# Optimization experiments

Hardware: AMD Instinct MI355X
Metric: run time of the kernel (lower is better)

## Reference

```python
import jax, jax.numpy as jnp
import numpy as np


def _fake_quant(x, num_bits):
    # Per-tensor uniform min/max fake quantization with STE (straight-through).
    qmax = float(2 ** num_bits - 1)
    mn = jnp.min(x)
    mx = jnp.max(x)
    scale = (mx - mn) / qmax
    q = jnp.round((x - mn) / scale) * scale + mn
    return x + jax.lax.stop_gradient(q - x)


def _qlinear(x, W, b, num_bits):
    xq = _fake_quant(x, num_bits)
    Wq = _fake_quant(W, num_bits)
    return xq @ Wq.T + b


def setup_inputs() -> dict:
    key = jax.random.key(0)
    ks = jax.random.split(key, 7)
    B, D, H = 8192, 1024, 1024
    s = 1.0 / np.sqrt(H)
    return {
        "input": jax.random.normal(ks[0], (B, D), jnp.float32),
        "h": jax.random.normal(ks[1], (B, H), jnp.float32),
        "c": jax.random.normal(ks[2], (B, H), jnp.float32),
        "W_in": jax.random.normal(ks[3], (4 * H, D), jnp.float32) * s,
        "b_in": jax.random.normal(ks[4], (4 * H,), jnp.float32) * s,
        "W_h": jax.random.normal(ks[5], (4 * H, H), jnp.float32) * s,
        "b_h": jax.random.normal(ks[6], (4 * H,), jnp.float32) * s,
        "num_bits": 8,
        "num_bits_grad": 8,
    }


def reference(input, h, c, W_in, b_in, W_h, b_h, num_bits, num_bits_grad):
    B = input.shape[0]
    Hd = h.shape[1]
    mixed_input = _qlinear(input, W_in, b_in, num_bits).reshape(B, 4, Hd)
    mixed_hidden = _qlinear(h, W_h, b_h, num_bits).reshape(B, 4, Hd)
    gates = mixed_input + mixed_hidden  # [B, 4, H]
    i = jax.nn.sigmoid(gates[:, 0, :])
    f = jax.nn.sigmoid(gates[:, 1, :])
    g = jnp.tanh(gates[:, 2, :])
    o = jax.nn.sigmoid(gates[:, 3, :])
    c_ = f * c + i * g
    h_ = o * jnp.tanh(c_)
    return (h_, c_)
```

## Files before the change

### kernel.cpp

```cpp
#include <hip/hip_runtime.h>
#include <hip/hip_bf16.h>

typedef unsigned short u16;
typedef int i32x4 __attribute__((ext_vector_type(4)));
typedef signed char s8;

#define NB_RED 256

__global__ void k_minmax_partial(const float* __restrict__ x, const float* __restrict__ h,
                                 const float* __restrict__ wi, const float* __restrict__ wh,
                                 float* __restrict__ partials) {
    int t = blockIdx.y;
    const float* p = (t == 0) ? x : (t == 1) ? h : (t == 2) ? wi : wh;
    int n4 = ((t < 2) ? (8192 * 1024) : (4096 * 1024)) >> 2;
    float mn = 3.4e38f, mx = -3.4e38f;
    const float4* p4 = (const float4*)p;
    for (int i = blockIdx.x * blockDim.x + threadIdx.x; i < n4; i += gridDim.x * blockDim.x) {
        float4 v = p4[i];
        mn = fminf(mn, fminf(fminf(v.x, v.y), fminf(v.z, v.w)));
        mx = fmaxf(mx, fmaxf(fmaxf(v.x, v.y), fmaxf(v.z, v.w)));
    }
    for (int d = 1; d < 64; d <<= 1) {
        mn = fminf(mn, __shfl_xor(mn, d));
        mx = fmaxf(mx, __shfl_xor(mx, d));
    }
    __shared__ float smn[4], smx[4];
    int wv = threadIdx.x >> 6;
    if ((threadIdx.x & 63) == 0) { smn[wv] = mn; smx[wv] = mx; }
    __syncthreads();
    if (threadIdx.x == 0) {
        mn = fminf(fminf(smn[0], smn[1]), fminf(smn[2], smn[3]));
        mx = fmaxf(fmaxf(smx[0], smx[1]), fmaxf(smx[2], smx[3]));
        partials[(t * NB_RED + blockIdx.x) * 2 + 0] = mn;
        partials[(t * NB_RED + blockIdx.x) * 2 + 1] = mx;
    }
}

__global__ void k_minmax_final(const float* __restrict__ partials, const int* __restrict__ nbits,
                               float* __restrict__ params) {
    int t = blockIdx.x;
    int tid = threadIdx.x;
    float mn = partials[(t * NB_RED + tid) * 2 + 0];
    float mx = partials[(t * NB_RED + tid) * 2 + 1];
    for (int d = 1; d < 64; d <<= 1) {
        mn = fminf(mn, __shfl_xor(mn, d));
        mx = fmaxf(mx, __shfl_xor(mx, d));
    }
    __shared__ float smn[4], smx[4];
    int wv = tid >> 6;
    if ((tid & 63) == 0) { smn[wv] = mn; smx[wv] = mx; }
    __syncthreads();
    if (tid == 0) {
        mn = fminf(fminf(smn[0], smn[1]), fminf(smn[2], smn[3]));
        mx = fmaxf(fmaxf(smx[0], smx[1]), fmaxf(smx[2], smx[3]));
        float qmax = (float)((1u << (*nbits)) - 1u);
        params[t * 2 + 0] = mn;
        params[t * 2 + 1] = (mx - mn) / qmax;
    }
}

static __device__ __forceinline__ int block_reduce_i(int v, int tid) {
    for (int d = 1; d < 64; d <<= 1) v += __shfl_xor(v, d);
    __shared__ int sred[4];
    if ((tid & 63) == 0) sred[tid >> 6] = v;
    __syncthreads();
    return sred[0] + sred[1] + sred[2] + sred[3];
}

__global__ void k_quant(const float* __restrict__ x, const float* __restrict__ h,
                        const float* __restrict__ wi, const float* __restrict__ wh,
                        const float* __restrict__ params,
                        const float* __restrict__ b_in, const float* __restrict__ b_h,
                        s8* __restrict__ A8, s8* __restrict__ W8,
                        float* __restrict__ Rax, float* __restrict__ Rah,
                        float* __restrict__ Rbi, float* __restrict__ Rbh,
                        float* __restrict__ bc) {
    int b = blockIdx.x;
    int t = threadIdx.x;
    if (b < 16384) {
        int tsel = b >> 13;
        int row = b & 8191;
        const float* src = tsel ? h : x;
        float mn = params[tsel * 2 + 0], s = params[tsel * 2 + 1];
        float4 v = ((const float4*)(src + (size_t)row * 1024))[t];
        int k0 = (int)fminf(255.f, fmaxf(0.f, rintf((v.x - mn) / s)));
        int k1 = (int)fminf(255.f, fmaxf(0.f, rintf((v.y - mn) / s)));
        int k2 = (int)fminf(255.f, fmaxf(0.f, rintf((v.z - mn) / s)));
        int k3 = (int)fminf(255.f, fmaxf(0.f, rintf((v.w - mn) / s)));
        unsigned p = ((unsigned)((k0 - 128) & 0xff)) | ((unsigned)((k1 - 128) & 0xff) << 8) |
                     ((unsigned)((k2 - 128) & 0xff) << 16) | ((unsigned)((k3 - 128) & 0xff) << 24);
        *(unsigned*)(A8 + (size_t)row * 2048 + tsel * 1024 + t * 4) = p;
        int sum = block_reduce_i(k0 + k1 + k2 + k3 - 512, t);
        if (t == 0) (tsel ? Rah : Rax)[row] = (float)sum;
    } else if (b < 24576) {
        int bb = b - 16384;
        int tsel = bb >> 12;
        int row = bb & 4095;
        const float* src = tsel ? wh : wi;
        float mn = params[(2 + tsel) * 2 + 0], s = params[(2 + tsel) * 2 + 1];
        int g = row >> 10, j = row & 1023;
        int prow = (j >> 4) * 64 + g * 16 + (j & 15);
        float4 v = ((const float4*)(src + (size_t)row * 1024))[t];
        int k0 = (int)fminf(255.f, fmaxf(0.f, rintf((v.x - mn) / s)));
        int k1 = (int)fminf(255.f, fmaxf(0.f, rintf((v.y - mn) / s)));
        int k2 = (int)fminf(255.f, fmaxf(0.f, rintf((v.z - mn) / s)));
        int k3 = (int)fminf(255.f, fmaxf(0.f, rintf((v.w - mn) / s)));
        unsigned p = ((unsigned)((k0 - 128) & 0xff)) | ((unsigned)((k1 - 128) & 0xff) << 8) |
                     ((unsigned)((k2 - 128) & 0xff) << 16) | ((unsigned)((k3 - 128) & 0xff) << 24);
        *(unsigned*)(W8 + (size_t)prow * 2048 + tsel * 1024 + t * 4) = p;
        int sum = block_reduce_i(k0 + k1 + k2 + k3 - 512, t);
        if (t == 0) (tsel ? Rbh : Rbi)[prow] = (float)sum;
    } else {
        int n = (b - 24576) * 256 + t;
        int j = (n >> 6) * 16 + (n & 15);
        int g = (n >> 4) & 3;
        bc[n] = b_in[g * 1024 + j] + b_h[g * 1024 + j];
    }
}

__global__ __launch_bounds__(256, 2) void k_gemm_lstm(
    const s8* __restrict__ A8, const s8* __restrict__ W8,
    const float* __restrict__ params, const float* __restrict__ bc,
    const float* __restrict__ Rax, const float* __restrict__ Rah,
    const float* __restrict__ Rbi, const float* __restrict__ Rbh,
    const float* __restrict__ c_in, float* __restrict__ out) {
    __shared__ __align__(16) s8 As[5][8192];
    __shared__ __align__(16) s8 Bs[5][8192];

    const int tid = threadIdx.x;
    const int wave = tid >> 6, lane = tid & 63;
    const int wr = wave >> 1, wc = wave & 1;
    const int la = lane & 15, hi = lane >> 4;

    const int bid = blockIdx.x;
    const int l = bid >> 3;
    const int bx = l >> 3;
    const int by = (bid & 7) * 8 + (l & 7);
    const int bm = by * 128, bn = bx * 128;

    const int srow = lane >> 2;
    const int skb = (((lane & 3) ^ ((srow >> 1) & 3)) * 16);
    const int fR = (la >> 1) & 3;

    const s8* pA0 = A8 + (size_t)(bm + wave * 16 + srow) * 2048 + skb;
    const s8* pA1 = pA0 + (size_t)64 * 2048;
    const s8* pB0 = W8 + (size_t)(bn + wave * 16 + srow) * 2048 + skb;
    const s8* pB1 = pB0 + (size_t)64 * 2048;

    i32x4 acc1[4][4], acc2[4][4];
#pragma unroll
    for (int m = 0; m < 4; m++)
#pragma unroll
        for (int n = 0; n < 4; n++) { acc1[m][n] = (i32x4)0; acc2[m][n] = (i32x4)0; }

#define STAGE(B, T)                                                                               \
    do {                                                                                          \
        __builtin_amdgcn_global_load_lds(                                                         \
            (const __attribute__((address_space(1))) void*)(pA0 + (T) * 64),                      \
            (__attribute__((address_space(3))) void*)&As[(B)][wave * 1024], 16, 0, 0);            \
        __builtin_amdgcn_global_load_lds(                                                         \
            (const __attribute__((address_space(1))) void*)(pA1 + (T) * 64),                      \
            (__attribute__((address_space(3))) void*)&As[(B)][(4 + wave) * 1024], 16, 0, 0);      \
        __builtin_amdgcn_global_load_lds(                                                         \
            (const __attribute__((address_space(1))) void*)(pB0 + (T) * 64),                      \
            (__attribute__((address_space(3))) void*)&Bs[(B)][wave * 1024], 16, 0, 0);            \
        __builtin_amdgcn_global_load_lds(                                                         \
            (const __attribute__((address_space(1))) void*)(pB1 + (T) * 64),                      \
            (__attribute__((address_space(3))) void*)&Bs[(B)][(4 + wave) * 1024], 16, 0, 0);      \
    } while (0)

#define COMPUTE(B, ACC)                                                                           \
    do {                                                                                          \
        i32x4 af[4], bf[4];                                                                       \
        _Pragma("unroll") for (int m = 0; m < 4; m++)                                             \
            af[m] = *(const i32x4*)&As[(B)][(wr * 64 + m * 16 + la) * 64 + ((hi ^ fR) * 16)];     \
        _Pragma("unroll") for (int n = 0; n < 4; n++)                                             \
            bf[n] = *(const i32x4*)&Bs[(B)][(wc * 64 + n * 16 + la) * 64 + ((hi ^ fR) * 16)];     \
        _Pragma("unroll") for (int m = 0; m < 4; m++)                                             \
            _Pragma("unroll") for (int n = 0; n < 4; n++)                                         \
                ACC[m][n] = __builtin_amdgcn_mfma_i32_16x16x64_i8(af[m], bf[n], ACC[m][n], 0, 0, 0); \
    } while (0)

    STAGE(0, 0);
    STAGE(1, 1);
    STAGE(2, 2);
    STAGE(3, 3);
    asm volatile("s_waitcnt vmcnt(12)" ::: "memory");
    __builtin_amdgcn_s_barrier();

#pragma unroll
    for (int t = 0; t < 32; ++t) {
        if (t < 28) STAGE((t + 4) % 5, t + 4);
        if (t < 16) COMPUTE(t % 5, acc1); else COMPUTE(t % 5, acc2);
        if (t < 28) { asm volatile("s_waitcnt vmcnt(12)" ::: "memory"); }
        else if (t == 28) { asm volatile("s_waitcnt vmcnt(8)" ::: "memory"); }
        else if (t == 29) { asm volatile("s_waitcnt vmcnt(4)" ::: "memory"); }
        else if (t == 30) { asm volatile("s_waitcnt vmcnt(0)" ::: "memory"); }
        if (t < 31) __builtin_amdgcn_s_barrier();
    }

#undef STAGE
#undef COMPUTE

    float mna = params[0], sa = params[1], mnh = params[2], sh = params[3];
    float mni = params[4], si = params[5], mnw = params[6], sw = params[7];
    float za = mna + 128.0f * sa, zi = mni + 128.0f * si;
    float zh = mnh + 128.0f * sh, zw = mnw + 128.0f * sw;
    float C0 = 1024.0f * (za * zi + zh * zw);
    float cax = sa * zi, cah = sh * zw;
    float cbx = si * za, cbh = sw * zh;
    float csx = sa * si, csh = sh * sw;

    const int nb = bn + wc * 64;
    float colt[4];
#pragma unroll
    for (int g = 0; g < 4; ++g) {
        int np = nb + g * 16 + la;
        colt[g] = bc[np] + cbx * Rbi[np] + cbh * Rbh[np] + C0;
    }
    const int ub = (nb >> 6) * 16 + la;

#pragma unroll
    for (int m = 0; m < 4; m++) {
#pragma unroll
        for (int q = 0; q < 4; q++) {
            int row = bm + wr * 64 + m * 16 + 4 * hi + q;
            float rterm = cax * Rax[row] + cah * Rah[row];
            float g0 = colt[0] + rterm + csx * (float)acc1[m][0][q] + csh * (float)acc2[m][0][q];
            float g1 = colt[1] + rterm + csx * (float)acc1[m][1][q] + csh * (float)acc2[m][1][q];
            float g2 = colt[2] + rterm + csx * (float)acc1[m][2][q] + csh * (float)acc2[m][2][q];
            float g3 = colt[3] + rterm + csx * (float)acc1[m][3][q] + csh * (float)acc2[m][3][q];
            float iv = 1.0f / (1.0f + __expf(-g0));
            float fv = 1.0f / (1.0f + __expf(-g1));
            float gv = tanhf(g2);
            float ov = 1.0f / (1.0f + __expf(-g3));
            size_t off = (size_t)row * 1024 + ub;
            float cv = c_in[off];
            float cn = fv * cv + iv * gv;
            float hn = ov * tanhf(cn);
            out[off] = hn;
            out[(size_t)8192 * 1024 + off] = cn;
        }
    }
}

extern "C" void kernel_launch(void* const* d_in, const int* in_sizes, int n_in,
                              void* d_out, int out_size, void* d_ws, size_t ws_size,
                              hipStream_t stream) {
    const float* x = (const float*)d_in[0];
    const float* h = (const float*)d_in[1];
    const float* c = (const float*)d_in[2];
    const float* wi = (const float*)d_in[3];
    const float* bi = (const float*)d_in[4];
    const float* wh = (const float*)d_in[5];
    const float* bh = (const float*)d_in[6];
    const int* nbits = (const int*)d_in[7];
    float* out = (float*)d_out;

    char* ws = (char*)d_ws;
    float* params   = (float*)ws;
    float* partials = (float*)(ws + 64);
    float* bc  = (float*)(ws + 16384);
    float* Rax = (float*)(ws + 32768);
    float* Rah = (float*)(ws + 65536);
    float* Rbi = (float*)(ws + 98304);
    float* Rbh = (float*)(ws + 114688);
    s8* A8 = (s8*)(ws + 131072);
    s8* W8 = (s8*)(ws + 131072 + (size_t)16 * 1024 * 1024);

    k_minmax_partial<<<dim3(NB_RED, 4), 256, 0, stream>>>(x, h, wi, wh, partials);
    k_minmax_final<<<4, 256, 0, stream>>>(partials, nbits, params);
    k_quant<<<24592, 256, 0, stream>>>(x, h, wi, wh, params, bi, bh,
                                       A8, W8, Rax, Rah, Rbi, Rbh, bc);
    k_gemm_lstm<<<2048, 256, 0, stream>>>(A8, W8, params, bc, Rax, Rah, Rbi, Rbh, c, out);
}
```

Measured before the change: 154.9 us.

## Merge dual accumulators via mid-loop rescale and shrink LDS ring for 3 blocks/CU

Replaces the two int32 accumulator sets (input GEMM and hidden GEMM) with one. Halfway through the K loop the accumulator is rescaled by the ratio of the two scale products and rounded, which halves accumulator registers. The LDS ring shrinks from 5 to 3 stages and launch bounds rise to 3 blocks per CU to raise occupancy. The costs are a shallower prefetch pipeline, and a rounding error from the int rescale that could affect accuracy.

After: 145.8 us. 1.06x faster.

```diff
diff --git a/kernel.cpp b/kernel.cpp
--- a/kernel.cpp
+++ b/kernel.cpp
@@ -118,14 +118,14 @@
     }
 }
 
-__global__ __launch_bounds__(256, 2) void k_gemm_lstm(
+__global__ __launch_bounds__(256, 3) void k_gemm_lstm(
     const s8* __restrict__ A8, const s8* __restrict__ W8,
     const float* __restrict__ params, const float* __restrict__ bc,
     const float* __restrict__ Rax, const float* __restrict__ Rah,
     const float* __restrict__ Rbi, const float* __restrict__ Rbh,
     const float* __restrict__ c_in, float* __restrict__ out) {
-    __shared__ __align__(16) s8 As[5][8192];
-    __shared__ __align__(16) s8 Bs[5][8192];
+    __shared__ __align__(16) s8 As[3][8192];
+    __shared__ __align__(16) s8 Bs[3][8192];
 
     const int tid = threadIdx.x;
     const int wave = tid >> 6, lane = tid & 63;
@@ -142,16 +142,20 @@
     const int skb = (((lane & 3) ^ ((srow >> 1) & 3)) * 16);
     const int fR = (la >> 1) & 3;
 
+    const float sa = params[1], sh = params[3], si = params[5], sw = params[7];
+    const float csx = sa * si, csh = sh * sw;
+    const float r = csx / csh;
+
     const s8* pA0 = A8 + (size_t)(bm + wave * 16 + srow) * 2048 + skb;
     const s8* pA1 = pA0 + (size_t)64 * 2048;
     const s8* pB0 = W8 + (size_t)(bn + wave * 16 + srow) * 2048 + skb;
     const s8* pB1 = pB0 + (size_t)64 * 2048;
 
-    i32x4 acc1[4][4], acc2[4][4];
+    i32x4 acc[4][4];
 #pragma unroll
     for (int m = 0; m < 4; m++)
 #pragma unroll
-        for (int n = 0; n < 4; n++) { acc1[m][n] = (i32x4)0; acc2[m][n] = (i32x4)0; }
+        for (int n = 0; n < 4; n++) acc[m][n] = (i32x4)0;
 
 #define STAGE(B, T)                                                                               \
     do {                                                                                          \
@@ -169,7 +173,7 @@
             (__attribute__((address_space(3))) void*)&Bs[(B)][(4 + wave) * 1024], 16, 0, 0);      \
     } while (0)
 
-#define COMPUTE(B, ACC)                                                                           \
+#define COMPUTE(B)                                                                                \
     do {                                                                                          \
         i32x4 af[4], bf[4];                                                                       \
         _Pragma("unroll") for (int m = 0; m < 4; m++)                                             \
@@ -178,23 +182,28 @@
             bf[n] = *(const i32x4*)&Bs[(B)][(wc * 64 + n * 16 + la) * 64 + ((hi ^ fR) * 16)];     \
         _Pragma("unroll") for (int m = 0; m < 4; m++)                                             \
             _Pragma("unroll") for (int n = 0; n < 4; n++)                                         \
-                ACC[m][n] = __builtin_amdgcn_mfma_i32_16x16x64_i8(af[m], bf[n], ACC[m][n], 0, 0, 0); \
+                acc[m][n] = __builtin_amdgcn_mfma_i32_16x16x64_i8(af[m], bf[n], acc[m][n], 0, 0, 0); \
     } while (0)
 
     STAGE(0, 0);
     STAGE(1, 1);
-    STAGE(2, 2);
-    STAGE(3, 3);
-    asm volatile("s_waitcnt vmcnt(12)" ::: "memory");
+    asm volatile("s_waitcnt vmcnt(4)" ::: "memory");
     __builtin_amdgcn_s_barrier();
 
 #pragma unroll
     for (int t = 0; t < 32; ++t) {
-        if (t < 28) STAGE((t + 4) % 5, t + 4);
-        if (t < 16) COMPUTE(t % 5, acc1); else COMPUTE(t % 5, acc2);
-        if (t < 28) { asm volatile("s_waitcnt vmcnt(12)" ::: "memory"); }
-        else if (t == 28) { asm volatile("s_waitcnt vmcnt(8)" ::: "memory"); }
-        else if (t == 29) { asm volatile("s_waitcnt vmcnt(4)" ::: "memory"); }
+        if (t < 30) STAGE((t + 2) % 3, t + 2);
+        if (t == 16) {
+#pragma unroll
+            for (int m = 0; m < 4; m++)
+#pragma unroll
+                for (int n = 0; n < 4; n++)
+#pragma unroll
+                    for (int q = 0; q < 4; q++)
+                        acc[m][n][q] = (int)rintf((float)acc[m][n][q] * r);
+        }
+        COMPUTE(t % 3);
+        if (t < 30) { asm volatile("s_waitcnt vmcnt(4)" ::: "memory"); }
         else if (t == 30) { asm volatile("s_waitcnt vmcnt(0)" ::: "memory"); }
         if (t < 31) __builtin_amdgcn_s_barrier();
     }
@@ -202,14 +211,12 @@
 #undef STAGE
 #undef COMPUTE
 
-    float mna = params[0], sa = params[1], mnh = params[2], sh = params[3];
-    float mni = params[4], si = params[5], mnw = params[6], sw = params[7];
+    float mna = params[0], mnh = params[2], mni = params[4], mnw = params[6];
     float za = mna + 128.0f * sa, zi = mni + 128.0f * si;
     float zh = mnh + 128.0f * sh, zw = mnw + 128.0f * sw;
     float C0 = 1024.0f * (za * zi + zh * zw);
     float cax = sa * zi, cah = sh * zw;
     float cbx = si * za, cbh = sw * zh;
-    float csx = sa * si, csh = sh * sw;
 
     const int nb = bn + wc * 64;
     float colt[4];
@@ -226,10 +233,10 @@
         for (int q = 0; q < 4; q++) {
             int row = bm + wr * 64 + m * 16 + 4 * hi + q;
             float rterm = cax * Rax[row] + cah * Rah[row];
-            float g0 = colt[0] + rterm + csx * (float)acc1[m][0][q] + csh * (float)acc2[m][0][q];
-            float g1 = colt[1] + rterm + csx * (float)acc1[m][1][q] + csh * (float)acc2[m][1][q];
-            float g2 = colt[2] + rterm + csx * (float)acc1[m][2][q] + csh * (float)acc2[m][2][q];
-            float g3 = colt[3] + rterm + csx * (float)acc1[m][3][q] + csh * (float)acc2[m][3][q];
+            float g0 = colt[0] + rterm + csh * (float)acc[m][0][q];
+            float g1 = colt[1] + rterm + csh * (float)acc[m][1][q];
+            float g2 = colt[2] + rterm + csh * (float)acc[m][2][q];
+            float g3 = colt[3] + rterm + csh * (float)acc[m][3][q];
             float iv = 1.0f / (1.0f + __expf(-g0));
             float fv = 1.0f / (1.0f + __expf(-g1));
             float gv = tanhf(g2);
```
